# Performance work log

Hardware: AMD Instinct MI355X
Metric: run time of the kernel (lower is better)

## Reference

```python
import jax, jax.numpy as jnp
import numpy as np

B, S, D, H = 4, 2048, 1024, 16
HD = D // H  # 64


def setup_inputs() -> dict:
    key = jax.random.key(0)
    ks = jax.random.split(key, 8)
    std = 0.02
    return {
        "input_tensor": jax.random.normal(ks[0], (B, S, D), jnp.float32),
        "attention_mask": jnp.zeros((B, 1, 1, S), jnp.float32),
        "Wq": jax.random.normal(ks[1], (D, D), jnp.float32) * std,
        "bq": jnp.zeros((D,), jnp.float32),
        "Wk": jax.random.normal(ks[2], (D, D), jnp.float32) * std,
        "bk": jnp.zeros((D,), jnp.float32),
        "Wv": jax.random.normal(ks[3], (D, D), jnp.float32) * std,
        "bv": jnp.zeros((D,), jnp.float32),
    }


def reference(input_tensor, attention_mask, Wq, bq, Wk, bk, Wv, bv):
    # QKV projections: [B,S,D]
    q = input_tensor @ Wq + bq
    k = input_tensor @ Wk + bk
    v = input_tensor @ Wv + bv
    # split heads -> [B,H,S,hd]
    split = lambda x: x.reshape(B, S, H, HD).transpose(0, 2, 1, 3)
    q, k, v = split(q), split(k), split(v)
    scale = HD ** (-0.5)
    # [B,H,S,S]
    scores = jnp.einsum("bhqd,bhkd->bhqk", q * scale, k) + attention_mask
    probs = jax.nn.softmax(scores, axis=-1)  # dropout skipped (train=False)
    out = jnp.einsum("bhqk,bhkd->bhqd", probs, v)
    return out.transpose(0, 2, 1, 3).reshape(B, S, D)
```

## Files before the change

kernel.cpp:

```cpp
#include <hip/hip_runtime.h>
#include <hip/hip_bf16.h>

#define BB 4
#define SS 2048
#define DD 1024
#define HH 16
#define HDD 64
#define MM (BB*SS)
#define KVB 64
#define NT (SS/KVB)

typedef __attribute__((ext_vector_type(4))) float f32x4;
typedef __attribute__((ext_vector_type(4))) _Float16 f16x4;
typedef __attribute__((ext_vector_type(8))) _Float16 f16x8;
typedef __attribute__((ext_vector_type(4))) unsigned int u32x4;

__device__ inline f32x4 mfma16(f16x8 a, f16x8 b, f32x4 c) {
  return __builtin_amdgcn_mfma_f32_16x16x32_f16(a, b, c, 0, 0, 0);
}

__device__ inline f16x8 comb(f16x4 lo, f16x4 hi) {
  return __builtin_shufflevector(lo, hi, 0, 1, 2, 3, 4, 5, 6, 7);
}

__device__ inline f16x8 ld_frag(const _Float16* p) {
  f16x4 lo = *reinterpret_cast<const f16x4*>(p);
  f16x4 hi = *reinterpret_cast<const f16x4*>(p + 16);
  return comb(lo, hi);
}

__global__ __launch_bounds__(256) void cvt_x_kernel(
    const float* __restrict__ x, _Float16* __restrict__ xh, int n4) {
  int i = blockIdx.x * 256 + threadIdx.x;
  int stride = gridDim.x * 256;
  for (; i < n4; i += stride) {
    f32x4 v = reinterpret_cast<const f32x4*>(x)[i];
    reinterpret_cast<f16x4*>(xh)[i] = __builtin_convertvector(v, f16x4);
  }
}

__global__ __launch_bounds__(256) void cvt_w_kernel(
    const float* __restrict__ Wq, const float* __restrict__ Wk,
    const float* __restrict__ Wv, _Float16* __restrict__ Wt) {
  __shared__ float tile[32][33];
  const int w = blockIdx.z;
  const float* W = (w == 0) ? Wq : (w == 1) ? Wk : Wv;
  _Float16* outp = Wt + (size_t)w * DD * DD;
  const int n0 = blockIdx.x * 32, k0 = blockIdx.y * 32;
  const int tx = threadIdx.x, ty = threadIdx.y;
#pragma unroll
  for (int i = 0; i < 32; i += 8)
    tile[ty + i][tx] = W[(size_t)(k0 + ty + i) * DD + n0 + tx];
  __syncthreads();
#pragma unroll
  for (int i = 0; i < 32; i += 8)
    outp[(size_t)(n0 + ty + i) * DD + k0 + tx] = (_Float16)tile[tx][ty + i];
}

#define LDT 40
__global__ __launch_bounds__(256) void qkv_gemm_kernel(
    const _Float16* __restrict__ Xh, const _Float16* __restrict__ Wt,
    const float* __restrict__ bq, const float* __restrict__ bk, const float* __restrict__ bv,
    _Float16* __restrict__ Qh, _Float16* __restrict__ Kh,
    _Float16* __restrict__ Vt) {
  __shared__ _Float16 At[128 * LDT];
  __shared__ _Float16 Bt[128 * LDT];
  const int w = blockIdx.y;
  const _Float16* Wp = Wt + (size_t)w * DD * DD;
  const int tid = threadIdx.x;
  const int lane = tid & 63, wave = tid >> 6;
  const int g = lane >> 4, r = lane & 15;
  const int mt = blockIdx.x & 63, nt = blockIdx.x >> 6;
  const int m0 = mt * 128, n0 = nt * 128;
  const int wr = wave >> 1, wc = wave & 1;

  f32x4 acc[4][4];
#pragma unroll
  for (int i = 0; i < 4; ++i)
#pragma unroll
    for (int j = 0; j < 4; ++j) { f32x4 z = {0.f, 0.f, 0.f, 0.f}; acc[i][j] = z; }

  const int r0 = tid >> 2, c0 = (tid & 3) * 8;
  const int r1 = (tid + 256) >> 2, c1 = (tid & 3) * 8;

  for (int kt = 0; kt < DD; kt += 32) {
    u32x4 a0 = *reinterpret_cast<const u32x4*>(&Xh[(size_t)(m0 + r0) * DD + kt + c0]);
    u32x4 a1 = *reinterpret_cast<const u32x4*>(&Xh[(size_t)(m0 + r1) * DD + kt + c1]);
    u32x4 b0 = *reinterpret_cast<const u32x4*>(&Wp[(size_t)(n0 + r0) * DD + kt + c0]);
    u32x4 b1 = *reinterpret_cast<const u32x4*>(&Wp[(size_t)(n0 + r1) * DD + kt + c1]);
    __syncthreads();
    *reinterpret_cast<u32x4*>(&At[r0 * LDT + c0]) = a0;
    *reinterpret_cast<u32x4*>(&At[r1 * LDT + c1]) = a1;
    *reinterpret_cast<u32x4*>(&Bt[r0 * LDT + c0]) = b0;
    *reinterpret_cast<u32x4*>(&Bt[r1 * LDT + c1]) = b1;
    __syncthreads();

    f16x8 af[4], bf[4];
#pragma unroll
    for (int ms = 0; ms < 4; ++ms)
      af[ms] = ld_frag(&At[(wr * 64 + ms * 16 + r) * LDT + 4 * g]);
#pragma unroll
    for (int ns = 0; ns < 4; ++ns)
      bf[ns] = ld_frag(&Bt[(wc * 64 + ns * 16 + r) * LDT + 4 * g]);
#pragma unroll
    for (int ms = 0; ms < 4; ++ms)
#pragma unroll
      for (int ns = 0; ns < 4; ++ns)
        acc[ms][ns] = mfma16(af[ms], bf[ns], acc[ms][ns]);
  }

  const float* bias = (w == 0) ? bq : (w == 1) ? bk : bv;
#pragma unroll
  for (int ns = 0; ns < 4; ++ns) {
    const int gcol = n0 + wc * 64 + ns * 16 + r;
    const float bv_ = bias[gcol];
    const int h = gcol >> 6, d = gcol & 63;
#pragma unroll
    for (int ms = 0; ms < 4; ++ms) {
#pragma unroll
      for (int reg = 0; reg < 4; ++reg) {
        const int grow = m0 + wr * 64 + ms * 16 + 4 * g + reg;
        const float v = acc[ms][ns][reg] + bv_;
        const int bb = grow >> 11, s = grow & 2047;
        const int bh = bb * HH + h;
        if (w == 0)
          Qh[((size_t)bh * SS + s) * HDD + d] = (_Float16)(v * 0.125f);
        else if (w == 1)
          Kh[((size_t)bh * SS + s) * HDD + d] = (_Float16)v;
        else
          Vt[((size_t)bh * HDD + d) * SS + s] = (_Float16)v;
      }
    }
  }
}

__global__ __launch_bounds__(256) void attn_kernel(
    const _Float16* __restrict__ Qh, const _Float16* __restrict__ Kh,
    const _Float16* __restrict__ Vg, const float* __restrict__ mask,
    float* __restrict__ out) {
  __shared__ _Float16 Ks[2][KVB * 64];
  __shared__ _Float16 Vs[2][KVB * 64];
  __shared__ float maskS[SS];
  const int bh = blockIdx.y;
  const int b = bh >> 4, h = bh & 15;
  const int tid = threadIdx.x, lane = tid & 63, wave = tid >> 6;
  const int g = lane >> 4, r = lane & 15;
  const int q0 = blockIdx.x * 128 + wave * 32;

  for (int i = tid; i < SS; i += 256) maskS[i] = mask[b * SS + i];

  f16x8 qf[2][2];
#pragma unroll
  for (int qs = 0; qs < 2; ++qs) {
    const _Float16* Qp = Qh + ((size_t)bh * SS + q0 + qs * 16 + r) * HDD;
    qf[qs][0] = *reinterpret_cast<const f16x8*>(Qp + 8 * g);
    qf[qs][1] = *reinterpret_cast<const f16x8*>(Qp + 32 + 8 * g);
  }

  float m_run[2] = {-1e30f, -1e30f}, l_run[2] = {0.f, 0.f};
  f32x4 acc[2][4];
#pragma unroll
  for (int qs = 0; qs < 2; ++qs)
#pragma unroll
    for (int i = 0; i < 4; ++i) { f32x4 z = {0.f, 0.f, 0.f, 0.f}; acc[qs][i] = z; }

  const _Float16* Kg = Kh + (size_t)bh * SS * HDD;
  const _Float16* Vgb = Vg + (size_t)bh * HDD * SS;

  const int srow = lane >> 3;
  const int scol = (lane & 7) * 8;
  u32x4 kreg[2], vreg[2];

  auto stage_load = [&](int kk) {
#pragma unroll
    for (int i = 0; i < 2; ++i) {
      const int row = wave * 16 + i * 8 + srow;
      kreg[i] = *reinterpret_cast<const u32x4*>(Kg + (size_t)(kk + row) * HDD + scol);
      vreg[i] = *reinterpret_cast<const u32x4*>(Vgb + (size_t)row * SS + kk + scol);
    }
  };
  auto stage_write = [&](int buf) {
#pragma unroll
    for (int i = 0; i < 2; ++i) {
      const int row = wave * 16 + i * 8 + srow;
      const int sw = (row & 7) << 3;
      *reinterpret_cast<u32x4*>(&Ks[buf][row * 64 + (scol ^ sw)]) = kreg[i];
      *reinterpret_cast<u32x4*>(&Vs[buf][row * 64 + (scol ^ sw)]) = vreg[i];
    }
  };

  int cur = 0;
  stage_load(0);
  stage_write(0);
  __syncthreads();

  for (int t = 0; t < NT; ++t) {
    const int kk = t * KVB;
    const bool more = (t + 1) < NT;
    if (more) stage_load(kk + KVB);

#pragma unroll
    for (int sg = 0; sg < 2; ++sg) {
      f32x4 st[2][2];
#pragma unroll
      for (int h16 = 0; h16 < 2; ++h16) {
        const int row = sg * 32 + h16 * 16 + r;
        const int sw = (row & 7) << 3;
        const _Float16* kb = &Ks[cur][row * 64];
        f16x8 a0 = *reinterpret_cast<const f16x8*>(kb + ((8 * g) ^ sw));
        f16x8 a1 = *reinterpret_cast<const f16x8*>(kb + ((32 + 8 * g) ^ sw));
        f32x4 z = {0.f, 0.f, 0.f, 0.f};
        st[0][h16] = mfma16(a1, qf[0][1], mfma16(a0, qf[0][0], z));
        st[1][h16] = mfma16(a1, qf[1][1], mfma16(a0, qf[1][0], z));
      }

      f16x8 pf[2];
#pragma unroll
      for (int qs = 0; qs < 2; ++qs) {
        float p0[4], p1[4];
        float tm = -1e30f;
#pragma unroll
        for (int j = 0; j < 4; ++j) {
          float s0 = st[qs][0][j] + maskS[kk + sg * 32 + 4 * g + j];
          float s1 = st[qs][1][j] + maskS[kk + sg * 32 + 16 + 4 * g + j];
          p0[j] = s0; p1[j] = s1;
          tm = fmaxf(tm, fmaxf(s0, s1));
        }
        tm = fmaxf(tm, __shfl_xor(tm, 16));
        tm = fmaxf(tm, __shfl_xor(tm, 32));
        const float m_new = fmaxf(m_run[qs], tm);
        const float corr = __expf(m_run[qs] - m_new);
        float rs = 0.f;
#pragma unroll
        for (int j = 0; j < 4; ++j) {
          p0[j] = __expf(p0[j] - m_new);
          p1[j] = __expf(p1[j] - m_new);
          rs += p0[j] + p1[j];
        }
        rs += __shfl_xor(rs, 16);
        rs += __shfl_xor(rs, 32);
        l_run[qs] = l_run[qs] * corr + rs;
        m_run[qs] = m_new;
#pragma unroll
        for (int i = 0; i < 4; ++i) acc[qs][i] = acc[qs][i] * corr;
        pf[qs] = f16x8{ (_Float16)p0[0], (_Float16)p0[1], (_Float16)p0[2], (_Float16)p0[3],
                        (_Float16)p1[0], (_Float16)p1[1], (_Float16)p1[2], (_Float16)p1[3] };
      }

#pragma unroll
      for (int dsb = 0; dsb < 4; ++dsb) {
        const int row = dsb * 16 + r;
        const int sw = (row & 7) << 3;
        const _Float16* vb = &Vs[cur][row * 64];
        f16x4 lo = *reinterpret_cast<const f16x4*>(vb + ((sg * 32 + 4 * g) ^ sw));
        f16x4 hi = *reinterpret_cast<const f16x4*>(vb + ((sg * 32 + 16 + 4 * g) ^ sw));
        f16x8 vf = comb(lo, hi);
        acc[0][dsb] = mfma16(vf, pf[0], acc[0][dsb]);
        acc[1][dsb] = mfma16(vf, pf[1], acc[1][dsb]);
      }
    }

    if (more) stage_write(cur ^ 1);
    __syncthreads();
    cur ^= 1;
  }

#pragma unroll
  for (int qs = 0; qs < 2; ++qs) {
    const float inv = 1.0f / l_run[qs];
    float* op = out + ((size_t)b * SS + q0 + qs * 16 + r) * DD + h * HDD;
#pragma unroll
    for (int dsb = 0; dsb < 4; ++dsb) {
      f32x4 o = { acc[qs][dsb][0] * inv, acc[qs][dsb][1] * inv,
                  acc[qs][dsb][2] * inv, acc[qs][dsb][3] * inv };
      *reinterpret_cast<f32x4*>(op + dsb * 16 + 4 * g) = o;
    }
  }
}

extern "C" void kernel_launch(void* const* d_in, const int* in_sizes, int n_in,
                              void* d_out, int out_size, void* d_ws, size_t ws_size,
                              hipStream_t stream) {
  const float* x    = (const float*)d_in[0];
  const float* mask = (const float*)d_in[1];
  const float* Wq   = (const float*)d_in[2];
  const float* bq   = (const float*)d_in[3];
  const float* Wk   = (const float*)d_in[4];
  const float* bk   = (const float*)d_in[5];
  const float* Wv   = (const float*)d_in[6];
  const float* bv   = (const float*)d_in[7];
  float* out = (float*)d_out;

  _Float16* Xh = (_Float16*)d_ws;
  _Float16* Wt = Xh + (size_t)MM * DD;
  _Float16* Qh = Wt + (size_t)3 * DD * DD;
  _Float16* Kh = Qh + (size_t)MM * DD;
  _Float16* Vt = Kh + (size_t)MM * DD;

  cvt_x_kernel<<<dim3(2048), dim3(256), 0, stream>>>(x, Xh, MM * DD / 4);
  cvt_w_kernel<<<dim3(32, 32, 3), dim3(32, 8), 0, stream>>>(Wq, Wk, Wv, Wt);
  qkv_gemm_kernel<<<dim3(512, 3), dim3(256), 0, stream>>>(Xh, Wt, bq, bk, bv, Qh, Kh, Vt);
  attn_kernel<<<dim3(SS / 128, BB * HH), dim3(256), 0, stream>>>(Qh, Kh, Vt, mask, out);
}
```

Before: 362.0 us.

## Use exp2 softmax with lazy rescaling, permuted V layout, and GEMM prefetch

Several changes at once. The Q scale and mask are premultiplied by log2(e) so the softmax can use exp2. The running max is only rescaled when a new score exceeds it by more than 8, and the row sum is reduced across lanes only once at the end. V is written in a permuted s-order so each PV fragment needs one 16-byte LDS read instead of two 8-byte reads, and probabilities are packed with cvt_pkrtz. Separately, the QKV GEMM prefetches the next K-slice of global data into registers while the current tile is being computed. The mask now comes from a new pre-scaling kernel and is read from global memory, which adds a launch and relies on extra workspace for the scaled mask.

```diff
diff --git a/kernel.cpp b/kernel.cpp
--- a/kernel.cpp
+++ b/kernel.cpp
@@ -11,9 +11,24 @@
 #define NT (SS/KVB)
 
 typedef __attribute__((ext_vector_type(4))) float f32x4;
+typedef __attribute__((ext_vector_type(2))) _Float16 f16x2;
 typedef __attribute__((ext_vector_type(4))) _Float16 f16x4;
 typedef __attribute__((ext_vector_type(8))) _Float16 f16x8;
+typedef __attribute__((ext_vector_type(2))) __fp16 fp16x2_builtin;
 typedef __attribute__((ext_vector_type(4))) unsigned int u32x4;
+
+#define LOG2E 1.4426950408889634f
+#define QSCALE (0.125f * LOG2E)
+
+__device__ inline float fast_exp2(float x) {
+  return __builtin_exp2f(x);
+}
+
+__device__ inline f16x2 pk2(float a, float b) {
+  union { fp16x2_builtin b2; f16x2 h2; } u;
+  u.b2 = __builtin_amdgcn_cvt_pkrtz(a, b);
+  return u.h2;
+}
 
 __device__ inline f32x4 mfma16(f16x8 a, f16x8 b, f32x4 c) {
   return __builtin_amdgcn_mfma_f32_16x16x32_f16(a, b, c, 0, 0, 0);
@@ -37,6 +52,12 @@
     f32x4 v = reinterpret_cast<const f32x4*>(x)[i];
     reinterpret_cast<f16x4*>(xh)[i] = __builtin_convertvector(v, f16x4);
   }
+}
+
+__global__ __launch_bounds__(256) void mask_scale_kernel(
+    const float* __restrict__ m, float* __restrict__ o, int n) {
+  int i = blockIdx.x * 256 + threadIdx.x;
+  if (i < n) o[i] = m[i] * LOG2E;
 }
 
 __global__ __launch_bounds__(256) void cvt_w_kernel(
@@ -83,11 +104,12 @@
   const int r0 = tid >> 2, c0 = (tid & 3) * 8;
   const int r1 = (tid + 256) >> 2, c1 = (tid & 3) * 8;
 
+  u32x4 a0 = *reinterpret_cast<const u32x4*>(&Xh[(size_t)(m0 + r0) * DD + c0]);
+  u32x4 a1 = *reinterpret_cast<const u32x4*>(&Xh[(size_t)(m0 + r1) * DD + c1]);
+  u32x4 b0 = *reinterpret_cast<const u32x4*>(&Wp[(size_t)(n0 + r0) * DD + c0]);
+  u32x4 b1 = *reinterpret_cast<const u32x4*>(&Wp[(size_t)(n0 + r1) * DD + c1]);
+
   for (int kt = 0; kt < DD; kt += 32) {
-    u32x4 a0 = *reinterpret_cast<const u32x4*>(&Xh[(size_t)(m0 + r0) * DD + kt + c0]);
-    u32x4 a1 = *reinterpret_cast<const u32x4*>(&Xh[(size_t)(m0 + r1) * DD + kt + c1]);
-    u32x4 b0 = *reinterpret_cast<const u32x4*>(&Wp[(size_t)(n0 + r0) * DD + kt + c0]);
-    u32x4 b1 = *reinterpret_cast<const u32x4*>(&Wp[(size_t)(n0 + r1) * DD + kt + c1]);
     __syncthreads();
     *reinterpret_cast<u32x4*>(&At[r0 * LDT + c0]) = a0;
     *reinterpret_cast<u32x4*>(&At[r1 * LDT + c1]) = a1;
@@ -95,6 +117,14 @@
     *reinterpret_cast<u32x4*>(&Bt[r1 * LDT + c1]) = b1;
     __syncthreads();
 
+    const bool more = (kt + 32) < DD;
+    if (more) {
+      a0 = *reinterpret_cast<const u32x4*>(&Xh[(size_t)(m0 + r0) * DD + kt + 32 + c0]);
+      a1 = *reinterpret_cast<const u32x4*>(&Xh[(size_t)(m0 + r1) * DD + kt + 32 + c1]);
+      b0 = *reinterpret_cast<const u32x4*>(&Wp[(size_t)(n0 + r0) * DD + kt + 32 + c0]);
+      b1 = *reinterpret_cast<const u32x4*>(&Wp[(size_t)(n0 + r1) * DD + kt + 32 + c1]);
+    }
+
     f16x8 af[4], bf[4];
 #pragma unroll
     for (int ms = 0; ms < 4; ++ms)
@@ -124,11 +154,16 @@
         const int bb = grow >> 11, s = grow & 2047;
         const int bh = bb * HH + h;
         if (w == 0)
-          Qh[((size_t)bh * SS + s) * HDD + d] = (_Float16)(v * 0.125f);
+          Qh[((size_t)bh * SS + s) * HDD + d] = (_Float16)(v * QSCALE);
         else if (w == 1)
           Kh[((size_t)bh * SS + s) * HDD + d] = (_Float16)v;
-        else
-          Vt[((size_t)bh * HDD + d) * SS + s] = (_Float16)v;
+        else {
+          const int w5 = s & 31;
+          const int pos = (w5 & 16) ? ((((w5 >> 2) & 3) << 3) + 4 + (w5 & 3))
+                                    : (((w5 >> 2) << 3) + (w5 & 3));
+          const int sp = (s & ~31) | pos;
+          Vt[((size_t)bh * HDD + d) * SS + sp] = (_Float16)v;
+        }
       }
     }
   }
@@ -136,19 +171,16 @@
 
 __global__ __launch_bounds__(256) void attn_kernel(
     const _Float16* __restrict__ Qh, const _Float16* __restrict__ Kh,
-    const _Float16* __restrict__ Vg, const float* __restrict__ mask,
+    const _Float16* __restrict__ Vg, const float* __restrict__ maskSc,
     float* __restrict__ out) {
   __shared__ _Float16 Ks[2][KVB * 64];
   __shared__ _Float16 Vs[2][KVB * 64];
-  __shared__ float maskS[SS];
   const int bh = blockIdx.y;
   const int b = bh >> 4, h = bh & 15;
   const int tid = threadIdx.x, lane = tid & 63, wave = tid >> 6;
   const int g = lane >> 4, r = lane & 15;
   const int q0 = blockIdx.x * 128 + wave * 32;
 
-  for (int i = tid; i < SS; i += 256) maskS[i] = mask[b * SS + i];
-
   f16x8 qf[2][2];
 #pragma unroll
   for (int qs = 0; qs < 2; ++qs) {
@@ -157,7 +189,8 @@
     qf[qs][1] = *reinterpret_cast<const f16x8*>(Qp + 32 + 8 * g);
   }
 
-  float m_run[2] = {-1e30f, -1e30f}, l_run[2] = {0.f, 0.f};
+  float m_run[2] = {-1e30f, -1e30f};
+  float l_run[2] = {0.f, 0.f};
   f32x4 acc[2][4];
 #pragma unroll
   for (int qs = 0; qs < 2; ++qs)
@@ -166,6 +199,7 @@
 
   const _Float16* Kg = Kh + (size_t)bh * SS * HDD;
   const _Float16* Vgb = Vg + (size_t)bh * HDD * SS;
+  const float* mbase = maskSc + b * SS;
 
   const int srow = lane >> 3;
   const int scol = (lane & 7) * 8;
@@ -198,6 +232,13 @@
     const int kk = t * KVB;
     const bool more = (t + 1) < NT;
     if (more) stage_load(kk + KVB);
+
+    f32x4 mk[2][2];
+#pragma unroll
+    for (int sg = 0; sg < 2; ++sg)
+#pragma unroll
+      for (int h16 = 0; h16 < 2; ++h16)
+        mk[sg][h16] = *reinterpret_cast<const f32x4*>(mbase + kk + sg * 32 + h16 * 16 + 4 * g);
 
 #pragma unroll
     for (int sg = 0; sg < 2; ++sg) {
@@ -218,43 +259,47 @@
 #pragma unroll
       for (int qs = 0; qs < 2; ++qs) {
         float p0[4], p1[4];
-        float tm = -1e30f;
+        float pmax = -1e30f;
 #pragma unroll
         for (int j = 0; j < 4; ++j) {
-          float s0 = st[qs][0][j] + maskS[kk + sg * 32 + 4 * g + j];
-          float s1 = st[qs][1][j] + maskS[kk + sg * 32 + 16 + 4 * g + j];
+          const float s0 = st[qs][0][j] + mk[sg][0][j];
+          const float s1 = st[qs][1][j] + mk[sg][1][j];
           p0[j] = s0; p1[j] = s1;
-          tm = fmaxf(tm, fmaxf(s0, s1));
+          pmax = fmaxf(pmax, fmaxf(s0, s1));
         }
-        tm = fmaxf(tm, __shfl_xor(tm, 16));
-        tm = fmaxf(tm, __shfl_xor(tm, 32));
-        const float m_new = fmaxf(m_run[qs], tm);
-        const float corr = __expf(m_run[qs] - m_new);
+        if (!__all(pmax <= m_run[qs] + 8.0f)) {
+          float tm = fmaxf(pmax, __shfl_xor(pmax, 16));
+          tm = fmaxf(tm, __shfl_xor(tm, 32));
+          const float m_new = fmaxf(m_run[qs], tm);
+          const float corr = fast_exp2(m_run[qs] - m_new);
+          l_run[qs] *= corr;
+#pragma unroll
+          for (int i = 0; i < 4; ++i) acc[qs][i] = acc[qs][i] * corr;
+          m_run[qs] = m_new;
+        }
+        const float mr = m_run[qs];
         float rs = 0.f;
 #pragma unroll
         for (int j = 0; j < 4; ++j) {
-          p0[j] = __expf(p0[j] - m_new);
-          p1[j] = __expf(p1[j] - m_new);
+          p0[j] = fast_exp2(p0[j] - mr);
+          p1[j] = fast_exp2(p1[j] - mr);
           rs += p0[j] + p1[j];
         }
-        rs += __shfl_xor(rs, 16);
-        rs += __shfl_xor(rs, 32);
-        l_run[qs] = l_run[qs] * corr + rs;
-        m_run[qs] = m_new;
-#pragma unroll
-        for (int i = 0; i < 4; ++i) acc[qs][i] = acc[qs][i] * corr;
-        pf[qs] = f16x8{ (_Float16)p0[0], (_Float16)p0[1], (_Float16)p0[2], (_Float16)p0[3],
-                        (_Float16)p1[0], (_Float16)p1[1], (_Float16)p1[2], (_Float16)p1[3] };
+        l_run[qs] += rs;
+        union { f16x2 h2[4]; f16x8 v; } u;
+        u.h2[0] = pk2(p0[0], p0[1]);
+        u.h2[1] = pk2(p0[2], p0[3]);
+        u.h2[2] = pk2(p1[0], p1[1]);
+        u.h2[3] = pk2(p1[2], p1[3]);
+        pf[qs] = u.v;
       }
 
 #pragma unroll
       for (int dsb = 0; dsb < 4; ++dsb) {
         const int row = dsb * 16 + r;
         const int sw = (row & 7) << 3;
-        const _Float16* vb = &Vs[cur][row * 64];
-        f16x4 lo = *reinterpret_cast<const f16x4*>(vb + ((sg * 32 + 4 * g) ^ sw));
-        f16x4 hi = *reinterpret_cast<const f16x4*>(vb + ((sg * 32 + 16 + 4 * g) ^ sw));
-        f16x8 vf = comb(lo, hi);
+        f16x8 vf = *reinterpret_cast<const f16x8*>(
+            &Vs[cur][row * 64 + ((sg * 32 + 8 * g) ^ sw)]);
         acc[0][dsb] = mfma16(vf, pf[0], acc[0][dsb]);
         acc[1][dsb] = mfma16(vf, pf[1], acc[1][dsb]);
       }
@@ -267,7 +312,10 @@
 
 #pragma unroll
   for (int qs = 0; qs < 2; ++qs) {
-    const float inv = 1.0f / l_run[qs];
+    float l = l_run[qs];
+    l += __shfl_xor(l, 16);
+    l += __shfl_xor(l, 32);
+    const float inv = 1.0f / l;
     float* op = out + ((size_t)b * SS + q0 + qs * 16 + r) * DD + h * HDD;
 #pragma unroll
     for (int dsb = 0; dsb < 4; ++dsb) {
@@ -296,9 +344,11 @@
   _Float16* Qh = Wt + (size_t)3 * DD * DD;
   _Float16* Kh = Qh + (size_t)MM * DD;
   _Float16* Vt = Kh + (size_t)MM * DD;
+  float* maskSc = (float*)(Vt + (size_t)MM * DD);
 
   cvt_x_kernel<<<dim3(2048), dim3(256), 0, stream>>>(x, Xh, MM * DD / 4);
+  mask_scale_kernel<<<dim3((BB * SS + 255) / 256), dim3(256), 0, stream>>>(mask, maskSc, BB * SS);
   cvt_w_kernel<<<dim3(32, 32, 3), dim3(32, 8), 0, stream>>>(Wq, Wk, Wv, Wt);
   qkv_gemm_kernel<<<dim3(512, 3), dim3(256), 0, stream>>>(Xh, Wt, bq, bk, bv, Qh, Kh, Vt);
-  attn_kernel<<<dim3(SS / 128, BB * HH), dim3(256), 0, stream>>>(Qh, Kh, Vt, mask, out);
-}
+  attn_kernel<<<dim3(SS / 128, BB * HH), dim3(256), 0, stream>>>(Qh, Kh, Vt, maskSc, out);
+}
```

Measured after the change: 340.9 us. 5.8% less time.
